# Optimization experiments

Measured on AMD Instinct MI355X. Metric: run time of the kernel, lower is better.

## Reference

```python
import jax, jax.numpy as jnp
import numpy as np

B = 4096
D = 128
TEMP = 0.5
EPS = 1e-8  # torch cosine_similarity norm clamp


def setup_inputs() -> dict:
    key = jax.random.key(0)
    k1, k2 = jax.random.split(key)
    zi = jax.random.normal(k1, (B, D), dtype=jnp.float32)
    zj = jax.random.normal(k2, (B, D), dtype=jnp.float32)
    return {"zi": zi, "zj": zj}


def reference(zi, zj):
    b = zi.shape[0]
    n2 = 2 * b
    z = jnp.concatenate([zi, zj], axis=0)                      # (2N, D)
    norm = jnp.maximum(jnp.linalg.norm(z, axis=-1, keepdims=True), EPS)
    zn = z / norm
    sim = zn @ zn.T                                            # (2N, 2N) cosine similarity
    # positives: torch.diag(sim, +B) and torch.diag(sim, -B)
    right = jnp.diagonal(sim, offset=b)                        # sim[i, i+B]
    left = jnp.diagonal(sim, offset=-b)                        # sim[i+B, i]
    pos = jnp.concatenate([left, right]) / TEMP                # (2N,)
    # logits row i = [pos_i] + all sims except self-diagonal and the positive,
    # so the softmax denominator set = all entries except the self-diagonal.
    logits = sim / TEMP
    neg_big = jnp.asarray(jnp.finfo(logits.dtype).min, logits.dtype)
    masked = jnp.where(jnp.eye(n2, dtype=bool), neg_big, logits)
    lse = jax.nn.logsumexp(masked, axis=1)                     # (2N,)
    # CrossEntropyLoss(reduction='sum') with label 0, then / 2N
    loss = jnp.sum(lse - pos) / n2
    return loss
```

## Files before the change

### kernel.cpp

```cpp
#include <hip/hip_runtime.h>
#include <hip/hip_bf16.h>


#define BB 4096
#define N2 8192
#define DD 128
#define CSPLIT 32
#define CW (N2 / CSPLIT)
#define NCT (CW / 16)

#define SCALE 1.69864360f

#if __has_builtin(__builtin_amdgcn_exp2f)
#define EXP2F(x) __builtin_amdgcn_exp2f(x)
#else
#define EXP2F(x) __expf((x) * 0.6931471805599453f)
#endif

using bf16 = __hip_bfloat16;
typedef __attribute__((ext_vector_type(8))) short short8;
typedef __attribute__((ext_vector_type(4))) float float4v;

__device__ __forceinline__ void gl_lds16(const char* g, char* ldst) {
  __builtin_amdgcn_global_load_lds(
      (const __attribute__((address_space(1))) void*)g,
      (__attribute__((address_space(3))) void*)ldst, 16, 0, 0);
}

__global__ __launch_bounds__(256) void ntx_norm_kernel(
    const float* __restrict__ zi, const float* __restrict__ zj,
    bf16* __restrict__ zn, float* __restrict__ rowsum, float* __restrict__ pos) {
  const int wave = threadIdx.x >> 6;
  const int lane = threadIdx.x & 63;
  const int pair = blockIdx.x * 4 + wave;
  float2 v = ((const float2*)(zi + (size_t)pair * DD))[lane];
  float2 w = ((const float2*)(zj + (size_t)pair * DD))[lane];
  float s1 = v.x * v.x + v.y * v.y;
  float s2 = w.x * w.x + w.y * w.y;
  float s3 = v.x * w.x + v.y * w.y;
  #pragma unroll
  for (int o = 32; o > 0; o >>= 1) {
    s1 += __shfl_xor(s1, o);
    s2 += __shfl_xor(s2, o);
    s3 += __shfl_xor(s3, o);
  }
  float nv = fmaxf(sqrtf(s1), 1e-8f);
  float nw = fmaxf(sqrtf(s2), 1e-8f);
  float rv = SCALE / nv, rw = SCALE / nw;
  bf16 bx = __float2bfloat16(v.x * rv);
  bf16 by = __float2bfloat16(v.y * rv);
  bf16 cx = __float2bfloat16(w.x * rw);
  bf16 cy = __float2bfloat16(w.y * rw);
  __hip_bfloat162 h2; h2.x = bx; h2.y = by;
  __hip_bfloat162 g2; g2.x = cx; g2.y = cy;
  ((__hip_bfloat162*)(zn + (size_t)pair * DD))[lane] = h2;
  ((__hip_bfloat162*)(zn + (size_t)(pair + BB) * DD))[lane] = g2;
  float fx = __bfloat162float(bx), fy = __bfloat162float(by);
  float gx = __bfloat162float(cx), gy = __bfloat162float(cy);
  float sii = fx * fx + fy * fy;
  float sjj = gx * gx + gy * gy;
  #pragma unroll
  for (int o = 32; o > 0; o >>= 1) {
    sii += __shfl_xor(sii, o);
    sjj += __shfl_xor(sjj, o);
  }
  if (lane == 0) {
    float c = s3 / (nv * nw);
    rowsum[pair]      = -EXP2F(sii);
    rowsum[pair + BB] = -EXP2F(sjj);
    pos[pair]      = c;
    pos[pair + BB] = c;
  }
}

__global__ __launch_bounds__(256) void ntx_sim_kernel(
    const bf16* __restrict__ zn, float* __restrict__ rowsum) {
  const int tid  = threadIdx.x;
  const int wave = tid >> 6;
  const int lane = tid & 63;
  const int quad = lane >> 4;
  const int l15  = lane & 15;
  const char* zb  = (const char*)zn;
  const short* zs = (const short*)zn;

  __shared__ float4 lds[2048];

  const int rowBase = blockIdx.y * 256 + wave * 64;
  const int colBase = blockIdx.x * CW;

  const int gr = lane >> 4;
  const int sl = lane & 15;
  const char* spE = zb + (size_t)(colBase + gr) * 256 + ((sl ^ gr) << 4);
  const char* spO = zb + (size_t)(colBase + gr) * 256 + ((sl ^ (4 + gr)) << 4);

  char* wb = (char*)lds + wave * 8192;

  gl_lds16(spE,        wb);
  gl_lds16(spO + 1024, wb + 1024);
  gl_lds16(spE + 2048, wb + 2048);
  gl_lds16(spO + 3072, wb + 3072);

  short8 a[4][4];
  #pragma unroll
  for (int t = 0; t < 4; t++) {
    const short* ap = zs + (size_t)(rowBase + t * 16 + l15) * DD + quad * 8;
    #pragma unroll
    for (int c = 0; c < 4; c++) a[t][c] = *(const short8*)(ap + c * 32);
  }
  asm volatile("" : "+v"(a[0][0]), "+v"(a[0][1]), "+v"(a[0][2]), "+v"(a[0][3]),
                    "+v"(a[1][0]), "+v"(a[1][1]), "+v"(a[1][2]), "+v"(a[1][3]),
                    "+v"(a[2][0]), "+v"(a[2][1]), "+v"(a[2][2]), "+v"(a[2][3]),
                    "+v"(a[3][0]), "+v"(a[3][1]), "+v"(a[3][2]), "+v"(a[3][3]));

  float rs[4][4];
  #pragma unroll
  for (int t = 0; t < 4; t++)
    #pragma unroll
    for (int r = 0; r < 4; r++) rs[t][r] = 0.0f;

  asm volatile("s_waitcnt vmcnt(0)" ::: "memory");
  __builtin_amdgcn_sched_barrier(0);

  #pragma unroll 1
  for (int rd = 0; rd < NCT; rd++) {
    const int cur = rd & 1;
    char* cb = wb + cur * 4096;

    if (rd + 1 < NCT) {
      const size_t ro = (size_t)(rd + 1) * 4096;
      char* nb = wb + (cur ^ 1) * 4096;
      gl_lds16(spE + ro,        nb);
      gl_lds16(spO + ro + 1024, nb + 1024);
      gl_lds16(spE + ro + 2048, nb + 2048);
      gl_lds16(spO + ro + 3072, nb + 3072);
    }

    short8 b[4];
    #pragma unroll
    for (int c = 0; c < 4; c++) {
      const int off = l15 * 256 + ((((c * 4 + quad)) ^ (l15 & 7)) << 4);
      b[c] = *(const short8*)(cb + off);
    }
    #pragma unroll
    for (int t = 0; t < 4; t++) {
      float4v acc = {0.f, 0.f, 0.f, 0.f};
      acc = __builtin_amdgcn_mfma_f32_16x16x32_bf16(a[t][0], b[0], acc, 0, 0, 0);
      acc = __builtin_amdgcn_mfma_f32_16x16x32_bf16(a[t][1], b[1], acc, 0, 0, 0);
      acc = __builtin_amdgcn_mfma_f32_16x16x32_bf16(a[t][2], b[2], acc, 0, 0, 0);
      acc = __builtin_amdgcn_mfma_f32_16x16x32_bf16(a[t][3], b[3], acc, 0, 0, 0);
      #pragma unroll
      for (int r = 0; r < 4; r++) rs[t][r] += EXP2F(acc[r]);
    }

    asm volatile("s_waitcnt vmcnt(0)" ::: "memory");
    __builtin_amdgcn_sched_barrier(0);
  }

  #pragma unroll
  for (int t = 0; t < 4; t++) {
    #pragma unroll
    for (int r = 0; r < 4; r++) {
      float s = rs[t][r];
      s += __shfl_xor(s, 1);
      s += __shfl_xor(s, 2);
      s += __shfl_xor(s, 4);
      s += __shfl_xor(s, 8);
      if (l15 == 0)
        atomicAdd(&rowsum[rowBase + t * 16 + quad * 4 + r], s);
    }
  }
}

__global__ __launch_bounds__(1024) void ntx_finalize_kernel(
    const float* __restrict__ rowsum, const float* __restrict__ pos,
    float* __restrict__ out) {
  float s = 0.f;
  for (int i = threadIdx.x; i < N2; i += 1024)
    s += __logf(rowsum[i]) - 2.0f * pos[i];
  #pragma unroll
  for (int o = 32; o > 0; o >>= 1) s += __shfl_xor(s, o);
  __shared__ float sm[16];
  const int wave = threadIdx.x >> 6;
  const int lane = threadIdx.x & 63;
  if (lane == 0) sm[wave] = s;
  __syncthreads();
  if (threadIdx.x == 0) {
    float t = 0.f;
    #pragma unroll
    for (int i = 0; i < 16; i++) t += sm[i];
    out[0] = t / (float)N2;
  }
}

extern "C" void kernel_launch(void* const* d_in, const int* in_sizes, int n_in,
                              void* d_out, int out_size, void* d_ws, size_t ws_size,
                              hipStream_t stream) {
  const float* zi = (const float*)d_in[0];
  const float* zj = (const float*)d_in[1];
  float* out = (float*)d_out;

  char* ws = (char*)d_ws;
  bf16* zn = (bf16*)ws;
  float* rowsum = (float*)(ws + (size_t)N2 * DD * 2);
  float* pos = rowsum + N2;

  ntx_norm_kernel<<<BB / 4, 256, 0, stream>>>(zi, zj, zn, rowsum, pos);
  dim3 grid(CSPLIT, N2 / 256);
  ntx_sim_kernel<<<grid, 256, 0, stream>>>(zn, rowsum);
  ntx_finalize_kernel<<<1, 1024, 0, stream>>>(rowsum, pos, out);
}
```

Before: 93.20 us.

## Store normalized embeddings in MFMA fragment layout and load B operands directly to registers

The norm kernel now shuffles each row's bf16 values and writes them in a pre-packed tile layout that matches the 16x16x32 MFMA operand fragments. The sim kernel drops the LDS staging and double buffering and loads both A and B fragments straight from global memory with coalesced 16-byte loads, prefetching the next tile into registers. This removes LDS traffic and the vmcnt barriers, but each wave now fetches B tiles from global/L2 on its own instead of sharing them through LDS. The prefetch on the last iteration wraps around to tile 0, which issues a redundant load.

```diff
diff --git a/kernel.cpp b/kernel.cpp
--- a/kernel.cpp
+++ b/kernel.cpp
@@ -21,15 +21,11 @@
 typedef __attribute__((ext_vector_type(8))) short short8;
 typedef __attribute__((ext_vector_type(4))) float float4v;
 
-__device__ __forceinline__ void gl_lds16(const char* g, char* ldst) {
-  __builtin_amdgcn_global_load_lds(
-      (const __attribute__((address_space(1))) void*)g,
-      (__attribute__((address_space(3))) void*)ldst, 16, 0, 0);
-}
 
 __global__ __launch_bounds__(256) void ntx_norm_kernel(
     const float* __restrict__ zi, const float* __restrict__ zj,
-    bf16* __restrict__ zn, float* __restrict__ rowsum, float* __restrict__ pos) {
+    char* __restrict__ znP, float* __restrict__ rowsum,
+    float* __restrict__ pos) {
   const int wave = threadIdx.x >> 6;
   const int lane = threadIdx.x & 63;
   const int pair = blockIdx.x * 4 + wave;
@@ -53,8 +49,26 @@
   bf16 cy = __float2bfloat16(w.y * rw);
   __hip_bfloat162 h2; h2.x = bx; h2.y = by;
   __hip_bfloat162 g2; g2.x = cx; g2.y = cy;
-  ((__hip_bfloat162*)(zn + (size_t)pair * DD))[lane] = h2;
-  ((__hip_bfloat162*)(zn + (size_t)(pair + BB) * DD))[lane] = g2;
+  unsigned hu = *(unsigned*)&h2;
+  unsigned gu = *(unsigned*)&g2;
+
+  const int i = lane & 15;
+  unsigned h0 = __shfl(hu, 4 * i + 0), g0 = __shfl(gu, 4 * i + 0);
+  unsigned h1 = __shfl(hu, 4 * i + 1), g1 = __shfl(gu, 4 * i + 1);
+  unsigned h2u = __shfl(hu, 4 * i + 2), g2u = __shfl(gu, 4 * i + 2);
+  unsigned h3 = __shfl(hu, 4 * i + 3), g3 = __shfl(gu, 4 * i + 3);
+  if (lane < 32) {
+    const int r = (lane < 16) ? pair : (pair + BB);
+    uint4 val;
+    val.x = (lane < 16) ? h0 : g0;
+    val.y = (lane < 16) ? h1 : g1;
+    val.z = (lane < 16) ? h2u : g2u;
+    val.w = (lane < 16) ? h3 : g3;
+    char* dst = znP + (((size_t)(r >> 4) * 4 + (i >> 2)) << 10) +
+                ((((i & 3) << 4) + (r & 15)) << 4);
+    *(uint4*)dst = val;
+  }
+
   float fx = __bfloat162float(bx), fy = __bfloat162float(by);
   float gx = __bfloat162float(cx), gy = __bfloat162float(cy);
   float sii = fx * fx + fy * fy;
@@ -74,39 +88,24 @@
 }
 
 __global__ __launch_bounds__(256) void ntx_sim_kernel(
-    const bf16* __restrict__ zn, float* __restrict__ rowsum) {
+    const char* __restrict__ znP, float* __restrict__ rowsum) {
   const int tid  = threadIdx.x;
   const int wave = tid >> 6;
   const int lane = tid & 63;
   const int quad = lane >> 4;
   const int l15  = lane & 15;
-  const char* zb  = (const char*)zn;
-  const short* zs = (const short*)zn;
-
-  __shared__ float4 lds[2048];
 
   const int rowBase = blockIdx.y * 256 + wave * 64;
-  const int colBase = blockIdx.x * CW;
-
-  const int gr = lane >> 4;
-  const int sl = lane & 15;
-  const char* spE = zb + (size_t)(colBase + gr) * 256 + ((sl ^ gr) << 4);
-  const char* spO = zb + (size_t)(colBase + gr) * 256 + ((sl ^ (4 + gr)) << 4);
-
-  char* wb = (char*)lds + wave * 8192;
-
-  gl_lds16(spE,        wb);
-  gl_lds16(spO + 1024, wb + 1024);
-  gl_lds16(spE + 2048, wb + 2048);
-  gl_lds16(spO + 3072, wb + 3072);
-
+  const int tile0   = blockIdx.x * NCT;
+
+  const int art = (rowBase >> 4);
   short8 a[4][4];
   #pragma unroll
-  for (int t = 0; t < 4; t++) {
-    const short* ap = zs + (size_t)(rowBase + t * 16 + l15) * DD + quad * 8;
-    #pragma unroll
-    for (int c = 0; c < 4; c++) a[t][c] = *(const short8*)(ap + c * 32);
-  }
+  for (int t = 0; t < 4; t++)
+    #pragma unroll
+    for (int c = 0; c < 4; c++)
+      a[t][c] = *(const short8*)(znP + (((size_t)(art + t) * 4 + c) << 10) +
+                                 lane * 16);
   asm volatile("" : "+v"(a[0][0]), "+v"(a[0][1]), "+v"(a[0][2]), "+v"(a[0][3]),
                     "+v"(a[1][0]), "+v"(a[1][1]), "+v"(a[1][2]), "+v"(a[1][3]),
                     "+v"(a[2][0]), "+v"(a[2][1]), "+v"(a[2][2]), "+v"(a[2][3]),
@@ -118,29 +117,22 @@
     #pragma unroll
     for (int r = 0; r < 4; r++) rs[t][r] = 0.0f;
 
-  asm volatile("s_waitcnt vmcnt(0)" ::: "memory");
-  __builtin_amdgcn_sched_barrier(0);
+  const char* bb = znP + ((size_t)tile0 << 12);
+
+  short8 b[4];
+  #pragma unroll
+  for (int c = 0; c < 4; c++)
+    b[c] = *(const short8*)(bb + (c << 10) + lane * 16);
 
   #pragma unroll 1
-  for (int rd = 0; rd < NCT; rd++) {
-    const int cur = rd & 1;
-    char* cb = wb + cur * 4096;
-
-    if (rd + 1 < NCT) {
-      const size_t ro = (size_t)(rd + 1) * 4096;
-      char* nb = wb + (cur ^ 1) * 4096;
-      gl_lds16(spE + ro,        nb);
-      gl_lds16(spO + ro + 1024, nb + 1024);
-      gl_lds16(spE + ro + 2048, nb + 2048);
-      gl_lds16(spO + ro + 3072, nb + 3072);
-    }
-
-    short8 b[4];
-    #pragma unroll
-    for (int c = 0; c < 4; c++) {
-      const int off = l15 * 256 + ((((c * 4 + quad)) ^ (l15 & 7)) << 4);
-      b[c] = *(const short8*)(cb + off);
-    }
+  for (int kt = 0; kt < NCT; kt++) {
+    const int nkt = (kt + 1) & (NCT - 1);
+    const char* bp = bb + ((size_t)nkt << 12);
+    short8 bn[4];
+    #pragma unroll
+    for (int c = 0; c < 4; c++)
+      bn[c] = *(const short8*)(bp + (c << 10) + lane * 16);
+
     #pragma unroll
     for (int t = 0; t < 4; t++) {
       float4v acc = {0.f, 0.f, 0.f, 0.f};
@@ -152,8 +144,8 @@
       for (int r = 0; r < 4; r++) rs[t][r] += EXP2F(acc[r]);
     }
 
-    asm volatile("s_waitcnt vmcnt(0)" ::: "memory");
-    __builtin_amdgcn_sched_barrier(0);
+    #pragma unroll
+    for (int c = 0; c < 4; c++) b[c] = bn[c];
   }
 
   #pragma unroll
@@ -200,12 +192,12 @@
   float* out = (float*)d_out;
 
   char* ws = (char*)d_ws;
-  bf16* zn = (bf16*)ws;
+  char* znP = ws;
   float* rowsum = (float*)(ws + (size_t)N2 * DD * 2);
   float* pos = rowsum + N2;
 
-  ntx_norm_kernel<<<BB / 4, 256, 0, stream>>>(zi, zj, zn, rowsum, pos);
+  ntx_norm_kernel<<<BB / 4, 256, 0, stream>>>(zi, zj, znP, rowsum, pos);
   dim3 grid(CSPLIT, N2 / 256);
-  ntx_sim_kernel<<<grid, 256, 0, stream>>>(zn, rowsum);
+  ntx_sim_kernel<<<grid, 256, 0, stream>>>(znP, rowsum);
   ntx_finalize_kernel<<<1, 1024, 0, stream>>>(rowsum, pos, out);
 }
```

Result: faster. 88.12 us, median of 2 (-5.5%).
